# Kernel optimization log

Hardware: AMD Instinct MI355X
Metric: run time of the kernel (lower is better)

## Reference

```python
import jax, jax.numpy as jnp
import numpy as np

LMAX = 6
NSH = (LMAX + 1) ** 2  # 49 spherical-harmonic coefficients
C = 128   # sphere_channels (num_resolutions=1 so sphere_channels_all == C)
H = 256   # hidden_channels
N = 4096  # nodes
RB, RA = 14, 13  # SO3 grid resolution (2*(lmax+1), 2*lmax+1)
EPS = 1e-5

_LIDX = np.concatenate([np.full(2 * l + 1, l) for l in range(LMAX + 1)])  # coeff -> l


def setup_inputs() -> dict:
    key = jax.random.key(0)
    ks = jax.random.split(key, 6)
    rn = lambda k, s, sc: jax.random.normal(k, s, jnp.float32) * sc
    return {
        "x": rn(ks[0], (N, NSH, C), 1.0),
        "ln0_w": jnp.ones((C,), jnp.float32),
        "ln0_b": jnp.zeros((C,), jnp.float32),
        "aff_w": jnp.ones((LMAX, C), jnp.float32),
        "w1": rn(ks[1], (LMAX + 1, H, C), C ** -0.5),
        "b1": jnp.zeros((H,), jnp.float32),
        "gate_w": rn(ks[2], (H, C), C ** -0.5),
        "gate_b": jnp.zeros((H,), jnp.float32),
        "w2": rn(ks[3], (LMAX + 1, C, H), H ** -0.5),
        "b2": jnp.zeros((C,), jnp.float32),
        "to_grid": rn(ks[4], (RB, RA, NSH), NSH ** -0.5),
        "from_grid": rn(ks[5], (RB, RA, NSH), (RB * RA) ** -0.5),
    }


def _balance_weight():
    # layer_norm_sh 'component' normalization with std_balance_degrees=True
    bal = np.zeros(NSH - 1, np.float32)
    for l in range(1, LMAX + 1):
        bal[l * l - 1 : l * l - 1 + 2 * l + 1] = 1.0 / (2 * l + 1)
    return jnp.asarray(bal / LMAX)


def reference(x, ln0_w, ln0_b, aff_w, w1, b1, gate_w, gate_b, w2, b2, to_grid, from_grid):
    # --- EquivariantLayerNormArraySphericalHarmonics ('layer_norm_sh') ---
    l0 = x[:, :1, :]                                   # [N,1,C]
    mu = jnp.mean(l0, axis=-1, keepdims=True)
    var = jnp.mean((l0 - mu) ** 2, axis=-1, keepdims=True)
    l0n = (l0 - mu) * jax.lax.rsqrt(var + EPS) * ln0_w + ln0_b
    rest = x[:, 1:, :]                                 # [N,48,C]
    fn = jnp.mean(jnp.einsum("nic,i->nc", rest * rest, _balance_weight()), axis=-1)  # [N]
    inv = jax.lax.rsqrt(fn + EPS)
    restn = rest * inv[:, None, None] * aff_w[_LIDX[1:] - 1]  # per-l affine weight
    xn = jnp.concatenate([l0n, restn], axis=1)          # [N,49,C]
    # --- gating linear on l=0 scalars ---
    gate = xn[:, :1, :] @ gate_w.T + gate_b             # [N,1,H]
    # --- SO3_LinearV2 #1 (block-diagonal per-l matmul, bias only on l=0) ---
    h = jnp.einsum("nmi,moi->nmo", xn, w1[_LIDX])      # [N,49,H]
    h = h.at[:, 0, :].add(b1)
    # --- S2Activation: SH -> grid, SiLU, grid -> SH ---
    g = jnp.einsum("bai,nic->nbac", to_grid, h)        # [N,RB,RA,H]
    g = jax.nn.silu(g)
    ht = jnp.einsum("bai,nbac->nic", from_grid, g)     # [N,49,H]
    # --- Separable: SiLU(scalars) for l=0, S2-activated for l>0 ---
    h2 = jnp.concatenate([jax.nn.silu(gate), ht[:, 1:, :]], axis=1)
    # --- SO3_LinearV2 #2 ---
    out = jnp.einsum("nmi,moi->nmo", h2, w2[_LIDX])    # [N,49,C]
    out = out.at[:, 0, :].add(b2)
    return out
```

## Files before the change

### kernel.cpp

```cpp
#include <hip/hip_runtime.h>
#include <stdint.h>

#define LMAXC 6
#define NSHC 49
#define CC 128
#define HH 256
#define NTOK 4096
#define NBA 182
#define EPSF 1e-5f

typedef __attribute__((ext_vector_type(8))) short bf16x8;
typedef __attribute__((ext_vector_type(4))) short s16x4;
typedef __attribute__((ext_vector_type(4))) float f32x4;

union U16x8 { uint4 v; ushort s[8]; };

__device__ __forceinline__ float bf2f(ushort u) {
  union { uint32_t i; float f; } w; w.i = ((uint32_t)u) << 16; return w.f;
}
__device__ __forceinline__ ushort f2bf(float f) {
  union { float f; uint32_t i; } w; w.f = f;
  uint32_t u = w.i;
  return (ushort)((u + 0x7fffu + ((u >> 16) & 1u)) >> 16);
}
__device__ __forceinline__ bf16x8 pack8(float4 a, float4 b) {
  bf16x8 r;
  r[0] = (short)f2bf(a.x); r[1] = (short)f2bf(a.y);
  r[2] = (short)f2bf(a.z); r[3] = (short)f2bf(a.w);
  r[4] = (short)f2bf(b.x); r[5] = (short)f2bf(b.y);
  r[6] = (short)f2bf(b.z); r[7] = (short)f2bf(b.w);
  return r;
}
__device__ __forceinline__ float siluf(float v) { return v / (1.f + __expf(-v)); }

__device__ __forceinline__ float block_sum(float v, volatile float* red, int t) {
  #pragma unroll
  for (int off = 32; off > 0; off >>= 1) v += __shfl_down(v, off, 64);
  __syncthreads();
  if ((t & 63) == 0) red[t >> 6] = v;
  __syncthreads();
  return red[0] + red[1] + red[2] + red[3];
}

__global__ __launch_bounds__(256) void k1_norm(
    const float* __restrict__ x, const float* __restrict__ ln0w,
    const float* __restrict__ ln0b, const float* __restrict__ affw,
    ushort* __restrict__ xn)
{
  __shared__ float red[4];
  int n = blockIdx.x, t = threadIdx.x;
  const float4* xv = (const float4*)(x + (size_t)n * NSHC * CC);
  ushort* xnp = xn + (size_t)n * NSHC * CC;
  float4 vals[7];
  float s0 = 0.f, s0q = 0.f, fq = 0.f;
  #pragma unroll
  for (int p = 0; p < 7; ++p) {
    int idx = p * 256 + t;
    if (idx < 1568) {
      float4 v = xv[idx];
      vals[p] = v;
      int m = idx >> 5;
      if (m == 0) {
        s0  += v.x + v.y + v.z + v.w;
        s0q += v.x*v.x + v.y*v.y + v.z*v.z + v.w*v.w;
      } else {
        int l = (int)sqrtf((float)m + 0.5f);
        float bw = 1.f / ((float)(2*l+1) * 6.f);
        fq += bw * (v.x*v.x + v.y*v.y + v.z*v.z + v.w*v.w);
      }
    }
  }
  float S0 = block_sum(s0, red, t);
  float S0Q = block_sum(s0q, red, t);
  float FQ = block_sum(fq, red, t);
  float mu = S0 * (1.f / 128.f);
  float var = S0Q * (1.f / 128.f) - mu * mu;
  float rstd = rsqrtf(var + EPSF);
  float inv = rsqrtf(FQ * (1.f / 128.f) + EPSF);
  #pragma unroll
  for (int p = 0; p < 7; ++p) {
    int idx = p * 256 + t;
    if (idx < 1568) {
      int m = idx >> 5, c0 = (idx & 31) * 4;
      float4 v = vals[p];
      float o[4];
      if (m == 0) {
        o[0] = (v.x - mu) * rstd * ln0w[c0+0] + ln0b[c0+0];
        o[1] = (v.y - mu) * rstd * ln0w[c0+1] + ln0b[c0+1];
        o[2] = (v.z - mu) * rstd * ln0w[c0+2] + ln0b[c0+2];
        o[3] = (v.w - mu) * rstd * ln0w[c0+3] + ln0b[c0+3];
      } else {
        int l = (int)sqrtf((float)m + 0.5f);
        const float* aw = affw + (size_t)(l - 1) * CC;
        o[0] = v.x * inv * aw[c0+0];
        o[1] = v.y * inv * aw[c0+1];
        o[2] = v.z * inv * aw[c0+2];
        o[3] = v.w * inv * aw[c0+3];
      }
      s16x4 pk;
      #pragma unroll
      for (int j = 0; j < 4; ++j) pk[j] = (short)f2bf(o[j]);
      *(s16x4*)&xnp[idx * 4] = pk;
    }
  }
}

__global__ __launch_bounds__(256) void k2_h(
    const ushort* __restrict__ xn, const float* __restrict__ w1,
    const float* __restrict__ b1, const float* __restrict__ gate_w,
    const float* __restrict__ gate_b, ushort* __restrict__ h,
    ushort* __restrict__ h2)
{
  extern __shared__ char smem[];
  ushort* sA = (ushort*)smem;
  ushort* sB = sA + 128 * 72;
  int* offs_tbl = (int*)(sB + 128 * 72);
  const int cum[9] = {0, 32, 128, 288, 512, 800, 1152, 1568, 1600};
  int bx = blockIdx.x, colbase = blockIdx.y * 128, t = threadIdx.x;
  int g = 0;
  #pragma unroll
  for (int k = 1; k < 8; ++k) if (bx >= cum[k]) g = k;
  int nb = bx - cum[g];
  bool isGate = (g == 7);
  int l = isGate ? 0 : g;
  int d = isGate ? 1 : (2 * l + 1);
  int mbase = isGate ? 0 : l * l;
  const float* wB = isGate ? gate_w : (w1 + (size_t)l * HH * CC);

  if (t < 128) {
    int r = nb * 128 + t;
    int nn = r / d;
    offs_tbl[t] = nn * NSHC + mbase + (r - nn * d);
  }
  __syncthreads();

  int wave = t >> 6, lane = t & 63, quad = lane >> 4, lan = lane & 15;
  int row0 = (wave >> 1) * 64, col0 = (wave & 1) * 64;
  f32x4 acc[4][4];
  f32x4 zf = {0.f, 0.f, 0.f, 0.f};
  #pragma unroll
  for (int a = 0; a < 4; ++a)
    #pragma unroll
    for (int b = 0; b < 4; ++b) acc[a][b] = zf;

  const uint4* xv = (const uint4*)xn;
  const float4* wv = (const float4*)wB;
  for (int kc = 0; kc < 2; ++kc) {
    #pragma unroll
    for (int p = 0; p < 4; ++p) {
      int idx = p * 256 + t, row = idx >> 3, c8 = idx & 7;
      *(uint4*)&sA[row * 72 + c8 * 8] = xv[(size_t)offs_tbl[row] * 16 + kc * 8 + c8];
    }
    #pragma unroll
    for (int p = 0; p < 4; ++p) {
      int idx = p * 256 + t, row = idx >> 3, c8 = idx & 7;
      size_t base = (size_t)(colbase + row) * 32 + kc * 16 + c8 * 2;
      *(bf16x8*)&sB[row * 72 + c8 * 8] = pack8(wv[base], wv[base + 1]);
    }
    __syncthreads();
    #pragma unroll
    for (int ks = 0; ks < 2; ++ks) {
      bf16x8 av[4], bv[4];
      #pragma unroll
      for (int mt = 0; mt < 4; ++mt)
        av[mt] = *(const bf16x8*)&sA[(row0 + mt*16 + lan) * 72 + ks*32 + quad*8];
      #pragma unroll
      for (int nt = 0; nt < 4; ++nt)
        bv[nt] = *(const bf16x8*)&sB[(col0 + nt*16 + lan) * 72 + ks*32 + quad*8];
      #pragma unroll
      for (int mt = 0; mt < 4; ++mt)
        #pragma unroll
        for (int nt = 0; nt < 4; ++nt)
          acc[mt][nt] = __builtin_amdgcn_mfma_f32_16x16x32_bf16(av[mt], bv[nt], acc[mt][nt], 0, 0, 0);
    }
    __syncthreads();
  }

  ushort* dst = isGate ? h2 : h;
  #pragma unroll
  for (int nt = 0; nt < 4; ++nt) {
    int o = colbase + col0 + nt * 16 + lan;
    float bias = 0.f;
    if (g == 0) bias = b1[o];
    if (isGate) bias = gate_b[o];
    #pragma unroll
    for (int mt = 0; mt < 4; ++mt) {
      int rb = row0 + mt * 16 + quad * 4;
      #pragma unroll
      for (int i = 0; i < 4; ++i) {
        float v = acc[mt][nt][i] + bias;
        if (isGate) v = siluf(v);
        dst[(size_t)offs_tbl[rb + i] * HH + o] = f2bf(v);
      }
    }
  }
}

__global__ __launch_bounds__(256) void k3_grid(
    const ushort* __restrict__ h, const float* __restrict__ tg,
    const float* __restrict__ fg, ushort* __restrict__ h2)
{
  extern __shared__ char smem[];
  ushort* sH = (ushort*)smem;
  ushort* sG = sH + 256 * 72;
  int t = threadIdx.x;
  int wave = t >> 6, lane = t & 63, quad = lane >> 4, lan = lane & 15;

  bf16x8 a1[3][2];
  {
    ushort* sc = sH;
    for (int i = t; i < 192 * 72; i += 256) sc[i] = 0;
    __syncthreads();
    for (int i = t; i < NBA * NSHC; i += 256) {
      int ba = i / NSHC, m = i - ba * NSHC;
      sc[ba * 72 + m] = f2bf(tg[i]);
    }
    __syncthreads();
    #pragma unroll
    for (int mt = 0; mt < 3; ++mt)
      #pragma unroll
      for (int ks = 0; ks < 2; ++ks)
        a1[mt][ks] = *(const bf16x8*)&sc[(wave*48 + mt*16 + lan) * 72 + ks*32 + quad*8];
    __syncthreads();
  }
  bf16x8 a2[6];
  {
    ushort* sc = sH;
    for (int i = t; i < 64 * 200; i += 256) sc[i] = 0;
    __syncthreads();
    for (int i = t; i < NBA * NSHC; i += 256) {
      int ba = i / NSHC, m = i - ba * NSHC;
      sc[m * 200 + ba] = f2bf(fg[i]);
    }
    __syncthreads();
    #pragma unroll
    for (int ks = 0; ks < 6; ++ks)
      a2[ks] = *(const bf16x8*)&sc[(wave*16 + lan) * 200 + ks*32 + quad*8];
    __syncthreads();
  }
  for (int i = t; i < 256 * 72; i += 256) sH[i] = 0;
  __syncthreads();

  f32x4 zf = {0.f, 0.f, 0.f, 0.f};
  for (int it = 0; it < 8; ++it) {
    int tok = blockIdx.x * 8 + it;
    const uint4* hv = (const uint4*)(h + (size_t)tok * NSHC * HH);
    for (int idx = t; idx < NSHC * 32; idx += 256) {
      int m = idx >> 5, o0 = (idx & 31) * 8;
      U16x8 u; u.v = hv[idx];
      #pragma unroll
      for (int j = 0; j < 8; ++j) sH[(o0 + j) * 72 + m] = u.s[j];
    }
    __syncthreads();

    for (int oc = 0; oc < 4; ++oc) {
      f32x4 acc1[3][4];
      #pragma unroll
      for (int a = 0; a < 3; ++a)
        #pragma unroll
        for (int b = 0; b < 4; ++b) acc1[a][b] = zf;
      #pragma unroll
      for (int ks = 0; ks < 2; ++ks) {
        bf16x8 bv[4];
        #pragma unroll
        for (int nt = 0; nt < 4; ++nt)
          bv[nt] = *(const bf16x8*)&sH[(oc*64 + nt*16 + lan) * 72 + ks*32 + quad*8];
        #pragma unroll
        for (int mt = 0; mt < 3; ++mt)
          #pragma unroll
          for (int nt = 0; nt < 4; ++nt)
            acc1[mt][nt] = __builtin_amdgcn_mfma_f32_16x16x32_bf16(a1[mt][ks], bv[nt], acc1[mt][nt], 0, 0, 0);
      }
      #pragma unroll
      for (int mt = 0; mt < 3; ++mt) {
        int ba0 = wave*48 + mt*16 + quad*4;
        #pragma unroll
        for (int nt = 0; nt < 4; ++nt) {
          int o_loc = nt*16 + lan;
          s16x4 pk;
          #pragma unroll
          for (int i = 0; i < 4; ++i) pk[i] = (short)f2bf(siluf(acc1[mt][nt][i]));
          *(s16x4*)&sG[o_loc * 200 + ba0] = pk;
        }
      }
      __syncthreads();
      f32x4 acc2[4];
      #pragma unroll
      for (int b = 0; b < 4; ++b) acc2[b] = zf;
      #pragma unroll
      for (int ks = 0; ks < 6; ++ks) {
        #pragma unroll
        for (int nt = 0; nt < 4; ++nt) {
          bf16x8 bv = *(const bf16x8*)&sG[(nt*16 + lan) * 200 + ks*32 + quad*8];
          acc2[nt] = __builtin_amdgcn_mfma_f32_16x16x32_bf16(a2[ks], bv, acc2[nt], 0, 0, 0);
        }
      }
      int mrow = wave * 16 + quad * 4;
      #pragma unroll
      for (int nt = 0; nt < 4; ++nt) {
        int o = oc * 64 + nt * 16 + lan;
        #pragma unroll
        for (int i = 0; i < 4; ++i) {
          int m = mrow + i;
          if (m >= 1 && m < NSHC)
            h2[((size_t)tok * NSHC + m) * HH + o] = f2bf(acc2[nt][i]);
        }
      }
      __syncthreads();
    }
  }
}

__global__ __launch_bounds__(256) void k4_out(
    const ushort* __restrict__ h2, const float* __restrict__ w2,
    const float* __restrict__ b2, float* __restrict__ out)
{
  extern __shared__ char smem[];
  ushort* sA = (ushort*)smem;
  ushort* sB = sA + 128 * 72;
  int* offs_tbl = (int*)(sB + 128 * 72);
  const int cum[8] = {0, 32, 128, 288, 512, 800, 1152, 1568};
  int bx = blockIdx.x, t = threadIdx.x;
  int g = 0;
  #pragma unroll
  for (int k = 1; k < 7; ++k) if (bx >= cum[k]) g = k;
  int nb = bx - cum[g];
  int l = g, d = 2*l+1, mbase = l*l;
  if (t < 128) {
    int r = nb * 128 + t;
    int nn = r / d;
    offs_tbl[t] = nn * NSHC + mbase + (r - nn * d);
  }
  __syncthreads();
  int wave = t >> 6, lane = t & 63, quad = lane >> 4, lan = lane & 15;
  int row0 = (wave >> 1) * 64, col0 = (wave & 1) * 64;
  f32x4 acc[4][4];
  f32x4 zf = {0.f, 0.f, 0.f, 0.f};
  #pragma unroll
  for (int a = 0; a < 4; ++a)
    #pragma unroll
    for (int b = 0; b < 4; ++b) acc[a][b] = zf;

  const uint4* av4 = (const uint4*)h2;
  const float4* wv = (const float4*)(w2 + (size_t)l * CC * HH);
  for (int kc = 0; kc < 4; ++kc) {
    #pragma unroll
    for (int p = 0; p < 4; ++p) {
      int idx = p * 256 + t, row = idx >> 3, c8 = idx & 7;
      *(uint4*)&sA[row * 72 + c8 * 8] = av4[(size_t)offs_tbl[row] * 32 + kc * 8 + c8];
    }
    #pragma unroll
    for (int p = 0; p < 4; ++p) {
      int idx = p * 256 + t, row = idx >> 3, c8 = idx & 7;
      size_t base = (size_t)row * 64 + kc * 16 + c8 * 2;
      *(bf16x8*)&sB[row * 72 + c8 * 8] = pack8(wv[base], wv[base + 1]);
    }
    __syncthreads();
    #pragma unroll
    for (int ks = 0; ks < 2; ++ks) {
      bf16x8 avf[4], bvf[4];
      #pragma unroll
      for (int mt = 0; mt < 4; ++mt)
        avf[mt] = *(const bf16x8*)&sA[(row0 + mt*16 + lan) * 72 + ks*32 + quad*8];
      #pragma unroll
      for (int nt = 0; nt < 4; ++nt)
        bvf[nt] = *(const bf16x8*)&sB[(col0 + nt*16 + lan) * 72 + ks*32 + quad*8];
      #pragma unroll
      for (int mt = 0; mt < 4; ++mt)
        #pragma unroll
        for (int nt = 0; nt < 4; ++nt)
          acc[mt][nt] = __builtin_amdgcn_mfma_f32_16x16x32_bf16(avf[mt], bvf[nt], acc[mt][nt], 0, 0, 0);
    }
    __syncthreads();
  }
  #pragma unroll
  for (int nt = 0; nt < 4; ++nt) {
    int c = col0 + nt * 16 + lan;
    float bias = (g == 0) ? b2[c] : 0.f;
    #pragma unroll
    for (int mt = 0; mt < 4; ++mt) {
      int rb = row0 + mt * 16 + quad * 4;
      #pragma unroll
      for (int i = 0; i < 4; ++i)
        out[(size_t)offs_tbl[rb + i] * CC + c] = acc[mt][nt][i] + bias;
    }
  }
}

extern "C" void kernel_launch(void* const* d_in, const int* in_sizes, int n_in,
                              void* d_out, int out_size, void* d_ws, size_t ws_size,
                              hipStream_t stream) {
  const float* x    = (const float*)d_in[0];
  const float* ln0w = (const float*)d_in[1];
  const float* ln0b = (const float*)d_in[2];
  const float* affw = (const float*)d_in[3];
  const float* w1   = (const float*)d_in[4];
  const float* b1   = (const float*)d_in[5];
  const float* gw   = (const float*)d_in[6];
  const float* gb   = (const float*)d_in[7];
  const float* w2   = (const float*)d_in[8];
  const float* b2   = (const float*)d_in[9];
  const float* tg   = (const float*)d_in[10];
  const float* fg   = (const float*)d_in[11];
  float* out = (float*)d_out;

  ushort* h = (ushort*)d_out;

  const size_t XN_BYTES = (size_t)NTOK * NSHC * CC * 2;
  char* ws = (char*)d_ws;
  ushort* xn = (ushort*)ws;
  ushort* h2 = (ushort*)(ws + XN_BYTES);

  const int LDS_GEMM = 2 * 128 * 72 * 2 + 128 * 4;
  const int LDS_GRID = (256 * 72 + 64 * 200) * 2;

  k1_norm<<<NTOK, 256, 0, stream>>>(x, ln0w, ln0b, affw, xn);
  k2_h<<<dim3(1600, 2), 256, LDS_GEMM, stream>>>(xn, w1, b1, gw, gb, h, h2);
  k3_grid<<<NTOK / 8, 256, LDS_GRID, stream>>>(h, tg, fg, h2);
  k4_out<<<1568, 256, LDS_GEMM, stream>>>(h2, w2, b2, out);
}
```

Measured before the change: 596.2 us.

## Store hidden activations transposed so grid kernel reads MFMA operands from global

```diff
diff --git a/kernel.cpp b/kernel.cpp
--- a/kernel.cpp
+++ b/kernel.cpp
@@ -8,6 +8,7 @@
 #define NTOK 4096
 #define NBA 182
 #define EPSF 1e-5f
+#define HTP 56
 
 typedef __attribute__((ext_vector_type(8))) short bf16x8;
 typedef __attribute__((ext_vector_type(4))) short s16x4;
@@ -45,10 +46,15 @@
 __global__ __launch_bounds__(256) void k1_norm(
     const float* __restrict__ x, const float* __restrict__ ln0w,
     const float* __restrict__ ln0b, const float* __restrict__ affw,
-    ushort* __restrict__ xn)
+    ushort* __restrict__ xn, ushort* __restrict__ h_t)
 {
   __shared__ float red[4];
   int n = blockIdx.x, t = threadIdx.x;
+  {
+    ushort* hp = h_t + (size_t)n * HH * HTP + (size_t)t * HTP;
+    #pragma unroll
+    for (int j = NSHC; j < HTP; ++j) hp[j] = 0;
+  }
   const float4* xv = (const float4*)(x + (size_t)n * NSHC * CC);
   ushort* xnp = xn + (size_t)n * NSHC * CC;
   float4 vals[7];
@@ -108,29 +114,32 @@
 __global__ __launch_bounds__(256) void k2_h(
     const ushort* __restrict__ xn, const float* __restrict__ w1,
     const float* __restrict__ b1, const float* __restrict__ gate_w,
-    const float* __restrict__ gate_b, ushort* __restrict__ h,
+    const float* __restrict__ gate_b, ushort* __restrict__ h_t,
     ushort* __restrict__ h2)
 {
   extern __shared__ char smem[];
   ushort* sA = (ushort*)smem;
   ushort* sB = sA + 128 * 72;
   int* offs_tbl = (int*)(sB + 128 * 72);
-  const int cum[9] = {0, 32, 128, 288, 512, 800, 1152, 1568, 1600};
+  const int off[9] = {0, 1, 4, 9, 16, 25, 36, 49, 50};
   int bx = blockIdx.x, colbase = blockIdx.y * 128, t = threadIdx.x;
+  int c = bx / 50, r = bx - c * 50;
   int g = 0;
   #pragma unroll
-  for (int k = 1; k < 8; ++k) if (bx >= cum[k]) g = k;
-  int nb = bx - cum[g];
+  for (int k = 1; k < 8; ++k) if (r >= off[k]) g = k;
+  int s = r - off[g];
   bool isGate = (g == 7);
   int l = isGate ? 0 : g;
   int d = isGate ? 1 : (2 * l + 1);
   int mbase = isGate ? 0 : l * l;
   const float* wB = isGate ? gate_w : (w1 + (size_t)l * HH * CC);
+  int nb = c * d + s;
 
   if (t < 128) {
-    int r = nb * 128 + t;
-    int nn = r / d;
-    offs_tbl[t] = nn * NSHC + mbase + (r - nn * d);
+    int rr = nb * 128 + t;
+    int nn = rr / d;
+    int mm = mbase + (rr - nn * d);
+    offs_tbl[t] = nn * 64 + mm;
   }
   __syncthreads();
 
@@ -149,7 +158,9 @@
     #pragma unroll
     for (int p = 0; p < 4; ++p) {
       int idx = p * 256 + t, row = idx >> 3, c8 = idx & 7;
-      *(uint4*)&sA[row * 72 + c8 * 8] = xv[(size_t)offs_tbl[row] * 16 + kc * 8 + c8];
+      int of = offs_tbl[row];
+      size_t xrow = (size_t)(of >> 6) * NSHC + (of & 63);
+      *(uint4*)&sA[row * 72 + c8 * 8] = xv[xrow * 16 + kc * 8 + c8];
     }
     #pragma unroll
     for (int p = 0; p < 4; ++p) {
@@ -176,7 +187,6 @@
     __syncthreads();
   }
 
-  ushort* dst = isGate ? h2 : h;
   #pragma unroll
   for (int nt = 0; nt < 4; ++nt) {
     int o = colbase + col0 + nt * 16 + lan;
@@ -189,69 +199,65 @@
       #pragma unroll
       for (int i = 0; i < 4; ++i) {
         float v = acc[mt][nt][i] + bias;
-        if (isGate) v = siluf(v);
-        dst[(size_t)offs_tbl[rb + i] * HH + o] = f2bf(v);
-      }
-    }
-  }
-}
-
-__global__ __launch_bounds__(256) void k3_grid(
-    const ushort* __restrict__ h, const float* __restrict__ tg,
+        int of = offs_tbl[rb + i];
+        if (isGate) {
+          h2[(size_t)(of >> 6) * (NSHC * HH) + o] = f2bf(siluf(v));
+        } else {
+          h_t[((size_t)(of >> 6) * HH + o) * HTP + (of & 63)] = f2bf(v);
+        }
+      }
+    }
+  }
+}
+
+__global__ __launch_bounds__(256, 3) void k3_grid(
+    const ushort* __restrict__ h_t, const float* __restrict__ tg,
     const float* __restrict__ fg, ushort* __restrict__ h2)
 {
-  extern __shared__ char smem[];
-  ushort* sH = (ushort*)smem;
-  ushort* sG = sH + 256 * 72;
+  __shared__ ushort sbuf[192 * 72];
   int t = threadIdx.x;
   int wave = t >> 6, lane = t & 63, quad = lane >> 4, lan = lane & 15;
 
   bf16x8 a1[3][2];
   {
-    ushort* sc = sH;
-    for (int i = t; i < 192 * 72; i += 256) sc[i] = 0;
+    for (int i = t; i < 192 * 72; i += 256) sbuf[i] = 0;
     __syncthreads();
     for (int i = t; i < NBA * NSHC; i += 256) {
       int ba = i / NSHC, m = i - ba * NSHC;
-      sc[ba * 72 + m] = f2bf(tg[i]);
+      sbuf[ba * 72 + m] = f2bf(tg[i]);
     }
     __syncthreads();
     #pragma unroll
     for (int mt = 0; mt < 3; ++mt)
       #pragma unroll
       for (int ks = 0; ks < 2; ++ks)
-        a1[mt][ks] = *(const bf16x8*)&sc[(wave*48 + mt*16 + lan) * 72 + ks*32 + quad*8];
+        a1[mt][ks] = *(const bf16x8*)&sbuf[(wave*48 + mt*16 + lan) * 72 + ks*32 + quad*8];
     __syncthreads();
   }
   bf16x8 a2[6];
   {
-    ushort* sc = sH;
-    for (int i = t; i < 64 * 200; i += 256) sc[i] = 0;
+    for (int i = t; i < 64 * 200; i += 256) sbuf[i] = 0;
     __syncthreads();
     for (int i = t; i < NBA * NSHC; i += 256) {
       int ba = i / NSHC, m = i - ba * NSHC;
-      sc[m * 200 + ba] = f2bf(fg[i]);
+      sbuf[m * 200 + ba] = f2bf(fg[i]);
     }
     __syncthreads();
     #pragma unroll
     for (int ks = 0; ks < 6; ++ks)
-      a2[ks] = *(const bf16x8*)&sc[(wave*16 + lan) * 200 + ks*32 + quad*8];
-    __syncthreads();
-  }
-  for (int i = t; i < 256 * 72; i += 256) sH[i] = 0;
-  __syncthreads();
+      a2[ks] = *(const bf16x8*)&sbuf[(wave*16 + lan) * 200 + ks*32 + quad*8];
+    __syncthreads();
+  }
+  ushort* sG = sbuf;
 
   f32x4 zf = {0.f, 0.f, 0.f, 0.f};
-  for (int it = 0; it < 8; ++it) {
-    int tok = blockIdx.x * 8 + it;
-    const uint4* hv = (const uint4*)(h + (size_t)tok * NSHC * HH);
-    for (int idx = t; idx < NSHC * 32; idx += 256) {
-      int m = idx >> 5, o0 = (idx & 31) * 8;
-      U16x8 u; u.v = hv[idx];
-      #pragma unroll
-      for (int j = 0; j < 8; ++j) sH[(o0 + j) * 72 + m] = u.s[j];
-    }
-    __syncthreads();
+  bf16x8 zb;
+  #pragma unroll
+  for (int j = 0; j < 8; ++j) zb[j] = 0;
+
+  for (int it = 0; it < 4; ++it) {
+    int tok = blockIdx.x * 4 + it;
+    const ushort* hp = h_t + (size_t)tok * HH * HTP;
 
     for (int oc = 0; oc < 4; ++oc) {
       f32x4 acc1[3][4];
@@ -261,10 +267,13 @@
         for (int b = 0; b < 4; ++b) acc1[a][b] = zf;
       #pragma unroll
       for (int ks = 0; ks < 2; ++ks) {
+        int kq = ks*32 + quad*8;
         bf16x8 bv[4];
         #pragma unroll
-        for (int nt = 0; nt < 4; ++nt)
-          bv[nt] = *(const bf16x8*)&sH[(oc*64 + nt*16 + lan) * 72 + ks*32 + quad*8];
+        for (int nt = 0; nt < 4; ++nt) {
+          int col = oc*64 + nt*16 + lan;
+          bv[nt] = (kq < HTP) ? *(const bf16x8*)(hp + (size_t)col * HTP + kq) : zb;
+        }
         #pragma unroll
         for (int mt = 0; mt < 3; ++mt)
           #pragma unroll
@@ -404,18 +413,17 @@
   const float* fg   = (const float*)d_in[11];
   float* out = (float*)d_out;
 
-  ushort* h = (ushort*)d_out;
+  ushort* h2 = (ushort*)d_out;
 
   const size_t XN_BYTES = (size_t)NTOK * NSHC * CC * 2;
   char* ws = (char*)d_ws;
-  ushort* xn = (ushort*)ws;
-  ushort* h2 = (ushort*)(ws + XN_BYTES);
+  ushort* xn  = (ushort*)ws;
+  ushort* h_t = (ushort*)(ws + XN_BYTES);
 
   const int LDS_GEMM = 2 * 128 * 72 * 2 + 128 * 4;
-  const int LDS_GRID = (256 * 72 + 64 * 200) * 2;
-
-  k1_norm<<<NTOK, 256, 0, stream>>>(x, ln0w, ln0b, affw, xn);
-  k2_h<<<dim3(1600, 2), 256, LDS_GEMM, stream>>>(xn, w1, b1, gw, gb, h, h2);
-  k3_grid<<<NTOK / 8, 256, LDS_GRID, stream>>>(h, tg, fg, h2);
+
+  k1_norm<<<NTOK, 256, 0, stream>>>(x, ln0w, ln0b, affw, xn, h_t);
+  k2_h<<<dim3(1600, 2), 256, LDS_GEMM, stream>>>(xn, w1, b1, gw, gb, h_t, h2);
+  k3_grid<<<NTOK / 4, 256, 0, stream>>>(h_t, tg, fg, h2);
   k4_out<<<1568, 256, LDS_GEMM, stream>>>(h2, w2, b2, out);
 }
```

Measured after the change: 650.6 us. 1.09x slower.

## Stage GEMM epilogues through LDS for coalesced stores, retune grid kernel

Applied to the files above, without the earlier changes.

```diff
diff --git a/kernel.cpp b/kernel.cpp
--- a/kernel.cpp
+++ b/kernel.cpp
@@ -12,8 +12,6 @@
 typedef __attribute__((ext_vector_type(8))) short bf16x8;
 typedef __attribute__((ext_vector_type(4))) short s16x4;
 typedef __attribute__((ext_vector_type(4))) float f32x4;
-
-union U16x8 { uint4 v; ushort s[8]; };
 
 __device__ __forceinline__ float bf2f(ushort u) {
   union { uint32_t i; float f; } w; w.i = ((uint32_t)u) << 16; return w.f;
@@ -114,6 +112,7 @@
   extern __shared__ char smem[];
   ushort* sA = (ushort*)smem;
   ushort* sB = sA + 128 * 72;
+  ushort* sE = (ushort*)smem;
   int* offs_tbl = (int*)(sB + 128 * 72);
   const int cum[9] = {0, 32, 128, 288, 512, 800, 1152, 1568, 1600};
   int bx = blockIdx.x, colbase = blockIdx.y * 128, t = threadIdx.x;
@@ -176,10 +175,10 @@
     __syncthreads();
   }
 
-  ushort* dst = isGate ? h2 : h;
   #pragma unroll
   for (int nt = 0; nt < 4; ++nt) {
-    int o = colbase + col0 + nt * 16 + lan;
+    int c = col0 + nt * 16 + lan;
+    int o = colbase + c;
     float bias = 0.f;
     if (g == 0) bias = b1[o];
     if (isGate) bias = gate_b[o];
@@ -190,66 +189,74 @@
       for (int i = 0; i < 4; ++i) {
         float v = acc[mt][nt][i] + bias;
         if (isGate) v = siluf(v);
-        dst[(size_t)offs_tbl[rb + i] * HH + o] = f2bf(v);
-      }
-    }
-  }
-}
-
-__global__ __launch_bounds__(256) void k3_grid(
+        sE[(rb + i) * 136 + c] = f2bf(v);
+      }
+    }
+  }
+  __syncthreads();
+  ushort* dst = isGate ? h2 : h;
+  #pragma unroll
+  for (int p = 0; p < 8; ++p) {
+    int idx = p * 256 + t, r = idx >> 4, cc = idx & 15;
+    bf16x8 vv = *(const bf16x8*)&sE[r * 136 + cc * 8];
+    *(bf16x8*)&dst[(size_t)offs_tbl[r] * HH + colbase + cc * 8] = vv;
+  }
+}
+
+__global__ __launch_bounds__(256, 2) void k3_grid(
     const ushort* __restrict__ h, const float* __restrict__ tg,
     const float* __restrict__ fg, ushort* __restrict__ h2)
 {
-  extern __shared__ char smem[];
-  ushort* sH = (ushort*)smem;
-  ushort* sG = sH + 256 * 72;
+  __shared__ ushort sH[256 * 72];
+  __shared__ ushort sG[64 * 200];
   int t = threadIdx.x;
   int wave = t >> 6, lane = t & 63, quad = lane >> 4, lan = lane & 15;
 
   bf16x8 a1[3][2];
   {
-    ushort* sc = sH;
-    for (int i = t; i < 192 * 72; i += 256) sc[i] = 0;
+    for (int i = t; i < 192 * 72; i += 256) sH[i] = 0;
     __syncthreads();
     for (int i = t; i < NBA * NSHC; i += 256) {
       int ba = i / NSHC, m = i - ba * NSHC;
-      sc[ba * 72 + m] = f2bf(tg[i]);
+      sH[ba * 72 + m] = f2bf(tg[i]);
     }
     __syncthreads();
     #pragma unroll
     for (int mt = 0; mt < 3; ++mt)
       #pragma unroll
       for (int ks = 0; ks < 2; ++ks)
-        a1[mt][ks] = *(const bf16x8*)&sc[(wave*48 + mt*16 + lan) * 72 + ks*32 + quad*8];
+        a1[mt][ks] = *(const bf16x8*)&sH[(wave*48 + mt*16 + lan) * 72 + ks*32 + quad*8];
     __syncthreads();
   }
   bf16x8 a2[6];
   {
-    ushort* sc = sH;
-    for (int i = t; i < 64 * 200; i += 256) sc[i] = 0;
+    for (int i = t; i < 64 * 200; i += 256) sG[i] = 0;
     __syncthreads();
     for (int i = t; i < NBA * NSHC; i += 256) {
       int ba = i / NSHC, m = i - ba * NSHC;
-      sc[m * 200 + ba] = f2bf(fg[i]);
+      sG[m * 200 + ba] = f2bf(fg[i]);
     }
     __syncthreads();
     #pragma unroll
     for (int ks = 0; ks < 6; ++ks)
-      a2[ks] = *(const bf16x8*)&sc[(wave*16 + lan) * 200 + ks*32 + quad*8];
-    __syncthreads();
-  }
-  for (int i = t; i < 256 * 72; i += 256) sH[i] = 0;
-  __syncthreads();
+      a2[ks] = *(const bf16x8*)&sG[(wave*16 + lan) * 200 + ks*32 + quad*8];
+    __syncthreads();
+  }
 
   f32x4 zf = {0.f, 0.f, 0.f, 0.f};
-  for (int it = 0; it < 8; ++it) {
-    int tok = blockIdx.x * 8 + it;
-    const uint4* hv = (const uint4*)(h + (size_t)tok * NSHC * HH);
-    for (int idx = t; idx < NSHC * 32; idx += 256) {
-      int m = idx >> 5, o0 = (idx & 31) * 8;
-      U16x8 u; u.v = hv[idx];
-      #pragma unroll
-      for (int j = 0; j < 8; ++j) sH[(o0 + j) * 72 + m] = u.s[j];
+
+  for (int it = 0; it < 4; ++it) {
+    int tok = blockIdx.x * 4 + it;
+    const ushort* hp = h + (size_t)tok * NSHC * HH;
+    #pragma unroll
+    for (int m0 = 0; m0 < 64; m0 += 8) {
+      bf16x8 w;
+      #pragma unroll
+      for (int j = 0; j < 8; ++j) {
+        int m = m0 + j;
+        w[j] = (m < NSHC) ? (short)hp[(size_t)m * HH + t] : (short)0;
+      }
+      *(bf16x8*)&sH[t * 72 + m0] = w;
     }
     __syncthreads();
 
@@ -261,10 +268,11 @@
         for (int b = 0; b < 4; ++b) acc1[a][b] = zf;
       #pragma unroll
       for (int ks = 0; ks < 2; ++ks) {
+        int kq = ks*32 + quad*8;
         bf16x8 bv[4];
         #pragma unroll
         for (int nt = 0; nt < 4; ++nt)
-          bv[nt] = *(const bf16x8*)&sH[(oc*64 + nt*16 + lan) * 72 + ks*32 + quad*8];
+          bv[nt] = *(const bf16x8*)&sH[(oc*64 + nt*16 + lan) * 72 + kq];
         #pragma unroll
         for (int mt = 0; mt < 3; ++mt)
           #pragma unroll
@@ -318,6 +326,7 @@
   extern __shared__ char smem[];
   ushort* sA = (ushort*)smem;
   ushort* sB = sA + 128 * 72;
+  float* sE = (float*)smem;
   int* offs_tbl = (int*)(sB + 128 * 72);
   const int cum[8] = {0, 32, 128, 288, 512, 800, 1152, 1568};
   int bx = blockIdx.x, t = threadIdx.x;
@@ -373,17 +382,31 @@
     }
     __syncthreads();
   }
-  #pragma unroll
-  for (int nt = 0; nt < 4; ++nt) {
-    int c = col0 + nt * 16 + lan;
-    float bias = (g == 0) ? b2[c] : 0.f;
-    #pragma unroll
-    for (int mt = 0; mt < 4; ++mt) {
-      int rb = row0 + mt * 16 + quad * 4;
-      #pragma unroll
-      for (int i = 0; i < 4; ++i)
-        out[(size_t)offs_tbl[rb + i] * CC + c] = acc[mt][nt][i] + bias;
-    }
+
+  #pragma unroll
+  for (int half = 0; half < 2; ++half) {
+    if ((wave >> 1) == half) {
+      #pragma unroll
+      for (int nt = 0; nt < 4; ++nt) {
+        int c = col0 + nt * 16 + lan;
+        float bias = (g == 0) ? b2[c] : 0.f;
+        #pragma unroll
+        for (int mt = 0; mt < 4; ++mt) {
+          int rr = mt * 16 + quad * 4;
+          #pragma unroll
+          for (int i = 0; i < 4; ++i)
+            sE[(rr + i) * 132 + c] = acc[mt][nt][i] + bias;
+        }
+      }
+    }
+    __syncthreads();
+    #pragma unroll
+    for (int p = 0; p < 8; ++p) {
+      int idx = p * 256 + t, r = idx >> 5, cc = idx & 31;
+      float4 v = *(const float4*)&sE[r * 132 + cc * 4];
+      *(float4*)&out[(size_t)offs_tbl[half * 64 + r] * CC + cc * 4] = v;
+    }
+    __syncthreads();
   }
 }
 
@@ -404,18 +427,17 @@
   const float* fg   = (const float*)d_in[11];
   float* out = (float*)d_out;
 
-  ushort* h = (ushort*)d_out;
+  ushort* h2 = (ushort*)d_out;
 
   const size_t XN_BYTES = (size_t)NTOK * NSHC * CC * 2;
   char* ws = (char*)d_ws;
   ushort* xn = (ushort*)ws;
-  ushort* h2 = (ushort*)(ws + XN_BYTES);
+  ushort* h  = (ushort*)(ws + XN_BYTES);
 
   const int LDS_GEMM = 2 * 128 * 72 * 2 + 128 * 4;
-  const int LDS_GRID = (256 * 72 + 64 * 200) * 2;
 
   k1_norm<<<NTOK, 256, 0, stream>>>(x, ln0w, ln0b, affw, xn);
   k2_h<<<dim3(1600, 2), 256, LDS_GEMM, stream>>>(xn, w1, b1, gw, gb, h, h2);
-  k3_grid<<<NTOK / 8, 256, LDS_GRID, stream>>>(h, tg, fg, h2);
+  k3_grid<<<NTOK / 4, 256, 0, stream>>>(h, tg, fg, h2);
   k4_out<<<1568, 256, LDS_GEMM, stream>>>(h2, w2, b2, out);
 }
```

After: 501.9 us. -15.8%, faster.
